# Optimization experiments

Hardware: AMD Instinct MI355X
Metric: run time of the kernel (lower is better)

The kernel has to match this reference:

```python
import jax, jax.numpy as jnp
import numpy as np

P1 = np.array([[1000.0, 0.0, 128.0, 64000.0],
               [0.0, 1000.0, 128.0, 64000.0],
               [0.0, 0.0, 1.0, 500.0]])
P2 = np.array([[-128.0, 0.0, 1000.0, 64000.0],
               [-128.0, 1000.0, 0.0, 64000.0],
               [-1.0, 0.0, 0.0, 500.0]])


def calculate_fundamental_matrix(P_src, P_dst):
    # l2 = F21 @ x1 : maps a point in P_src onto a line in P_dst
    C1 = -np.linalg.inv(P_src[:3, :3]) @ P_src[:3, 3]
    e = P_dst @ np.append(C1, 1.0)          # epipole of src camera center in dst view
    return np.cross(e, np.eye(3) * -1) @ P_dst @ np.linalg.pinv(P_src)


def setup_inputs() -> dict:
    key = jax.random.key(0)
    view1 = jax.random.normal(key, (8, 4, 256, 256), dtype=jnp.float32)
    F21 = calculate_fundamental_matrix(P1, P2).astype(np.float32)
    return {"view1": view1, "F": jnp.asarray(F21)}


def reference(view1, F):
    """Epipolar image translation: out(x2) = line integral of view1 along the
    epipolar line l1 = F^T @ x2 (bilinear sampling in v, unit steps in u,
    zero outside the image). Matches fume_torch_lib.translate semantics."""
    B, C, H, W = view1.shape
    dt = view1.dtype
    F = F.astype(dt)
    ys = jnp.arange(H, dtype=dt)[:, None]   # (H,1)
    xs = jnp.arange(W, dtype=dt)[None, :]   # (1,W)
    # line coefficients l = F^T @ [x, y, 1], per output pixel -> (H,W)
    a = F[0, 0] * xs + F[1, 0] * ys + F[2, 0]
    b = F[0, 1] * xs + F[1, 1] * ys + F[2, 1]
    c = F[0, 2] * xs + F[1, 2] * ys + F[2, 2]
    n = jnp.sqrt(a * a + b * b) + jnp.asarray(1e-12, dt)
    a, b, c = a / n, b / n, c / n
    ok = (jnp.abs(b) > 1e-6).astype(dt)                 # drop near-vertical lines
    b_safe = jnp.where(jnp.abs(b) > 1e-6, b, jnp.asarray(1.0, dt))

    def step(acc, u):
        uf = u.astype(dt)
        v = -(a * uf + c) / b_safe                      # (H,W) source row per out pixel
        v0 = jnp.floor(v)
        f = v - v0
        i0 = v0.astype(jnp.int32)
        i1 = i0 + 1
        m0 = ((i0 >= 0) & (i0 < H)).astype(dt)
        m1 = ((i1 >= 0) & (i1 < H)).astype(dt)
        col = jax.lax.dynamic_index_in_dim(view1, u, axis=3, keepdims=False)  # (B,C,H)
        s0 = col[:, :, jnp.clip(i0, 0, H - 1)]          # (B,C,H,W)
        s1 = col[:, :, jnp.clip(i1, 0, H - 1)]
        val = (s0 * (1.0 - f) * m0 + s1 * f * m1) * ok
        return acc + val, None

    out, _ = jax.lax.scan(step, jnp.zeros_like(view1), jnp.arange(W))
    return out
```

## Files before the change

### kernel.cpp

```cpp
#include <hip/hip_runtime.h>
#include <cstdint>

constexpr int Hh = 256, Ww = 256, BCc = 32;

constexpr int RBLK = 35;
constexpr int USTRIDE = RBLK * BCc * 8 * 2;
constexpr int UPLANES = 264;

constexpr int DW2    = 140;
constexpr int UROW2  = DW2 * BCc * 4;
constexpr size_t PSIZE = (size_t)UPLANES * UROW2;
constexpr size_t T5_BYTES = 2 * PSIZE;

typedef _Float16 half2v   __attribute__((ext_vector_type(2)));
typedef _Float16 half8v   __attribute__((ext_vector_type(8)));
typedef __fp16   fp16x2   __attribute__((ext_vector_type(2)));
typedef float    float16v __attribute__((ext_vector_type(16)));
typedef float    float4v  __attribute__((ext_vector_type(4)));
typedef uint32_t uint4v   __attribute__((ext_vector_type(4)));

static __device__ inline half2v pack2(float a, float b) {
    fp16x2 r = __builtin_amdgcn_cvt_pkrtz(a, b);
    return __builtin_bit_cast(half2v, r);
}

__global__ __launch_bounds__(256) void fume_pack2(const float* __restrict__ in,
                                                  char* __restrict__ P) {
    const int t   = threadIdx.x;
    const int bid = blockIdx.x;
    const int rt  = bid % 18;
    const int ut  = bid / 18;
    const int R0  = rt * 16;
    const int u0  = ut * 16;
    __shared__ float lds[32][17][17];

    for (int idx = t; idx < 32 * 17 * 4; idx += 256) {
        int q   = idx & 3;
        int rem = idx >> 2;
        int rl  = rem % 17;
        int ch  = rem / 17;
        int r   = R0 + rl - 8;
        int uq  = u0 + q * 4;
        float4v v = {0.f, 0.f, 0.f, 0.f};
        if ((unsigned)r < 256u && uq < 256)
            v = *(const float4v*)&in[ch * (Hh * Ww) + r * Ww + uq];
        lds[ch][rl][q * 4 + 0] = v[0];
        lds[ch][rl][q * 4 + 1] = v[1];
        lds[ch][rl][q * 4 + 2] = v[2];
        lds[ch][rl][q * 4 + 3] = v[3];
    }
    __syncthreads();

    for (int w = t; w < 8192; w += 256) {
        int ch    = w & 31;
        int rest  = w >> 5;
        int uu    = rest & 15;
        int rest2 = rest >> 4;
        int dd    = rest2 & 7;
        int p     = rest2 >> 3;
        int d     = (R0 >> 1) + dd;
        int u     = u0 + uu;
        if (d >= DW2 || u >= UPLANES) continue;
        int rl = 2 * dd + p;
        half2v pr = pack2(lds[ch][rl][uu], lds[ch][rl + 1][uu]);
        uint32_t wv;
        __builtin_memcpy(&wv, &pr, 4);
        *(uint32_t*)(P + (size_t)p * PSIZE + (size_t)u * UROW2
                     + d * 128 + ch * 4) = wv;
    }
}

__global__ __launch_bounds__(256, 8) void fume_mfma3(const char* __restrict__ P,
                                                     const float* __restrict__ Fm,
                                                     float* __restrict__ out) {
    __shared__ float red[4][32][33];
    const int t    = threadIdx.x;
    const int lane = t & 63;
    const int wq   = t >> 6;
    const int px   = lane & 31;
    const int h    = lane >> 5;
    const int bid  = (int)blockIdx.x;
    const int idx8 = bid >> 3;
    const int y    = ((bid & 7) << 5) + (idx8 >> 3);
    const int x0   = (idx8 & 7) * 32;
    const int x    = x0 + px;

    float xf = (float)x, yf = (float)y;
    float a = Fm[0] * xf + Fm[3] * yf + Fm[6];
    float b = Fm[1] * xf + Fm[4] * yf + Fm[7];
    float c = Fm[2] * xf + Fm[5] * yf + Fm[8];
    float n = sqrtf(a * a + b * b) + 1e-12f;
    a /= n; b /= n; c /= n;

    float alpha, beta_i;
    int u_lo, u_hi;
    if (fabsf(b) > 1e-6f) {
        alpha  = -a / b;
        beta_i = -c / b + 8.f;
        u_lo = 0; u_hi = Ww - 1;
        if (fabsf(alpha) > 1e-12f) {
            float inv = 1.f / alpha;
            float t0 = (7.f - beta_i) * inv;
            float t1 = (264.f - beta_i) * inv;
            int lo = (int)floorf(fminf(t0, t1));
            int hi = (int)ceilf (fmaxf(t0, t1));
            u_lo = lo > 0 ? lo : 0;
            u_hi = hi < (Ww - 1) ? hi : (Ww - 1);
        } else if (beta_i <= 7.f || beta_i >= 264.f) {
            u_lo = 1 << 20; u_hi = -(1 << 20);
        }
    } else {
        alpha = 0.f; beta_i = 3.0e4f;
        u_lo = 1 << 20; u_hi = -(1 << 20);
    }

    float xA = (float)x0, xB = (float)(x0 + 31);
    float aA = Fm[0] * xA + Fm[3] * yf + Fm[6];
    float bA = Fm[1] * xA + Fm[4] * yf + Fm[7];
    float cA = Fm[2] * xA + Fm[5] * yf + Fm[8];
    float aB = Fm[0] * xB + Fm[3] * yf + Fm[6];
    float bB = Fm[1] * xB + Fm[4] * yf + Fm[7];
    float cB = Fm[2] * xB + Fm[5] * yf + Fm[8];
    float alA = -aA / bA, beA = -cA / bA + 8.f;
    float alB = -aB / bB, beB = -cB / bB + 8.f;

    int lo = u_lo, hi = u_hi;
#pragma unroll
    for (int off = 1; off < 64; off <<= 1) {
        int l2 = __shfl_xor(lo, off, 64);
        int h2 = __shfl_xor(hi, off, 64);
        lo = lo < l2 ? lo : l2;
        hi = hi > h2 ? hi : h2;
    }
    lo = __builtin_amdgcn_readfirstlane(lo);
    hi = __builtin_amdgcn_readfirstlane(hi);

    float16v acc = {0.f, 0.f, 0.f, 0.f, 0.f, 0.f, 0.f, 0.f,
                    0.f, 0.f, 0.f, 0.f, 0.f, 0.f, 0.f, 0.f};

    if (lo <= hi) {
        int len = hi - lo + 1;
        int C   = (len + 3) >> 2;
        int cq  = (C + 3) >> 2;
        int nit = C - wq * cq;
        nit = nit < 0 ? 0 : (nit > cq ? cq : nit);
        int us  = lo + wq * cq * 4;

        int   u_l = us + lane;
        float uf  = (float)u_l;
        float vAl = fmaf(alA, uf, beA);
        float vBl = fmaf(alB, uf, beB);
        float mnu = fminf(vAl, vBl);
        float Mff = floorf(mnu - 0.01f);
        Mff = fmaxf(0.f, fminf(Mff, 272.f));
        int   Mi   = (int)Mff;
        int   pb   = Mi & 1;
        int   vOff = (pb ? (int)PSIZE : 0) + u_l * UROW2 + (Mi >> 1) * 128;
        int   vMfB = __builtin_bit_cast(int, Mff);

        float alpha2 = alpha + alpha;
        float vhh = fmaf(alpha, (float)(us + h), beta_i);
        const int chb = px << 2;

        uint32_t bA8[8], bB8[8], bC8[8];

#define FUME_ISS3(BUF, CH)                                                    \
    do {                                                                      \
        _Pragma("unroll")                                                     \
        for (int pr_ = 0; pr_ < 2; ++pr_) {                                   \
            int li_  = (CH) * 4 + 2 * pr_;                                    \
            int oe_  = __builtin_amdgcn_readlane(vOff, li_);                  \
            int oo_  = __builtin_amdgcn_readlane(vOff, li_ + 1);              \
            int sel_ = h ? oo_ : oe_;                                         \
            const char* q_ = P + (unsigned)(sel_ + chb);                      \
            _Pragma("unroll")                                                 \
            for (int k_ = 0; k_ < 4; ++k_)                                    \
                (BUF)[4 * pr_ + k_] = *(const uint32_t*)(q_ + 128 * k_);      \
        }                                                                     \
    } while (0)

#define FUME_COMP3(BUF, CH)                                                   \
    do {                                                                      \
        _Pragma("unroll")                                                     \
        for (int pr_ = 0; pr_ < 2; ++pr_) {                                   \
            int li_ = (CH) * 4 + 2 * pr_;                                     \
            int me_ = __builtin_amdgcn_readlane(vMfB, li_);                   \
            int mo_ = __builtin_amdgcn_readlane(vMfB, li_ + 1);               \
            float mf_ = __builtin_bit_cast(float, h ? mo_ : me_);             \
            float vbl_ = vhh - mf_;                                           \
            uint32_t aw_[4];                                                  \
            _Pragma("unroll")                                                 \
            for (int j_ = 0; j_ < 4; ++j_) {                                  \
                float d0_ = vbl_ - (float)(2 * j_);                           \
                float d1_ = vbl_ - (float)(2 * j_ + 1);                       \
                float t0_ = fmaxf(0.f, 1.f - fabsf(d0_));                     \
                float t1_ = fmaxf(0.f, 1.f - fabsf(d1_));                     \
                half2v tj_ = pack2(t0_, t1_);                                 \
                __builtin_memcpy(&aw_[j_], &tj_, 4);                          \
            }                                                                 \
            half8v A_;                                                        \
            __builtin_memcpy(&A_, aw_, 16);                                   \
            uint4v bw_ = {(BUF)[4 * pr_ + 0], (BUF)[4 * pr_ + 1],             \
                          (BUF)[4 * pr_ + 2], (BUF)[4 * pr_ + 3]};            \
            half8v B_ = __builtin_bit_cast(half8v, bw_);                      \
            acc = __builtin_amdgcn_mfma_f32_32x32x16_f16(A_, B_, acc, 0, 0, 0);\
            vhh += alpha2;                                                    \
        }                                                                     \
    } while (0)

        if (nit > 0) {
            FUME_ISS3(bA8, 0);
            if (nit > 1) FUME_ISS3(bB8, 1);
            int cc = 0;
            while (cc + 3 <= nit) {
                FUME_ISS3(bC8, cc + 2);
                FUME_COMP3(bA8, cc);
                int pf1 = (cc + 3 < nit) ? cc + 3 : nit - 1;
                FUME_ISS3(bA8, pf1);
                FUME_COMP3(bB8, cc + 1);
                int pf2 = (cc + 4 < nit) ? cc + 4 : nit - 1;
                FUME_ISS3(bB8, pf2);
                FUME_COMP3(bC8, cc + 2);
                cc += 3;
            }
            if (cc < nit) FUME_COMP3(bA8, cc);
            if (cc + 1 < nit) FUME_COMP3(bB8, cc + 1);
        }
#undef FUME_ISS3
#undef FUME_COMP3
    }

#pragma unroll
    for (int r = 0; r < 16; ++r) {
        int m = (r & 3) + 8 * (r >> 2) + 4 * h;
        red[wq][m][px] = acc[r];
    }
    __syncthreads();
    {
        int pxs = t & 31, cg = t >> 5;
#pragma unroll
        for (int jj = 0; jj < 4; ++jj) {
            int ch = cg + 8 * jj;
            float val = red[0][pxs][ch] + red[1][pxs][ch]
                      + red[2][pxs][ch] + red[3][pxs][ch];
            out[(size_t)ch * (Hh * Ww) + y * Ww + x0 + pxs] = val;
        }
    }
}

__global__ __launch_bounds__(256) void fume_pack(const float* __restrict__ in,
                                                 char* __restrict__ T4) {
    const int t   = threadIdx.x;
    const int bid = blockIdx.x;
    if (bid >= 512) {
        constexpr int NA = UPLANES * 3 * 32;
        constexpr int NB = 8 * 32 * 32;
        for (int id = (bid - 512) * 256 + t; id < NA + NB; id += 8 * 256) {
            int u, blk, ch;
            if (id < NA) {
                u = id / 96;
                int rem = id - u * 96;
                int bsel = rem >> 5;
                blk = (bsel == 0) ? 0 : (bsel == 1 ? 33 : 34);
                ch = rem & 31;
            } else {
                int id2 = id - NA;
                u = 256 + (id2 >> 10);
                int rem = id2 & 1023;
                blk = 1 + (rem >> 5);
                ch = rem & 31;
            }
            uint4v z = {0, 0, 0, 0};
            *(uint4v*)(T4 + (size_t)u * USTRIDE + blk * 512 + ch * 16) = z;
        }
        return;
    }
    __shared__ float lds[8][8][65];
    const int chg = bid & 3;
    const int r0  = ((bid >> 2) & 31) * 8;
    const int u0  = (bid >> 7) * 64;
    const int blk = (r0 >> 3) + 1;

#pragma unroll
    for (int it = 0; it < 16; ++it) {
        int idx = it * 256 + t;
        int ch = idx >> 9, rr = (idx >> 6) & 7, uu = idx & 63;
        lds[ch][rr][uu] =
            in[(chg * 8 + ch) * (Hh * Ww) + (r0 + rr) * Ww + u0 + uu];
    }
    __syncthreads();
    const int chl = t & 7;
#pragma unroll
    for (int p = 0; p < 2; ++p) {
        int u_l = (t >> 3) + p * 32;
        uint32_t w[4];
#pragma unroll
        for (int j = 0; j < 4; ++j) {
            half2v pr = pack2(lds[chl][2 * j][u_l], lds[chl][2 * j + 1][u_l]);
            __builtin_memcpy(&w[j], &pr, 4);
        }
        uint4v val = {w[0], w[1], w[2], w[3]};
        *(uint4v*)(T4 + (size_t)(u0 + u_l) * USTRIDE + blk * 512
                   + (chg * 8 + chl) * 16) = val;
    }
}

__global__ __launch_bounds__(256, 4) void fume_mfma(const char* __restrict__ T4,
                                                    const float* __restrict__ Fm,
                                                    float* __restrict__ out) {
    __shared__ float red[4][32][33];
    const int t    = threadIdx.x;
    const int lane = t & 63;
    const int wq   = t >> 6;
    const int px   = lane & 31;
    const int h    = lane >> 5;
    const int bid  = (int)blockIdx.x;
    const int idx8 = bid >> 3;
    const int y    = ((bid & 7) << 5) + (idx8 >> 3);
    const int x0   = (idx8 & 7) * 32;
    const int x    = x0 + px;

    float xf = (float)x, yf = (float)y;
    float a = Fm[0] * xf + Fm[3] * yf + Fm[6];
    float b = Fm[1] * xf + Fm[4] * yf + Fm[7];
    float c = Fm[2] * xf + Fm[5] * yf + Fm[8];
    float n = sqrtf(a * a + b * b) + 1e-12f;
    a /= n; b /= n; c /= n;

    float alpha, beta_i;
    int u_lo, u_hi;
    if (fabsf(b) > 1e-6f) {
        alpha  = -a / b;
        beta_i = -c / b + 8.f;
        u_lo = 0; u_hi = Ww - 1;
        if (fabsf(alpha) > 1e-12f) {
            float inv = 1.f / alpha;
            float t0 = (7.f - beta_i) * inv;
            float t1 = (264.f - beta_i) * inv;
            int lo = (int)floorf(fminf(t0, t1));
            int hi = (int)ceilf (fmaxf(t0, t1));
            u_lo = lo > 0 ? lo : 0;
            u_hi = hi < (Ww - 1) ? hi : (Ww - 1);
        } else if (beta_i <= 7.f || beta_i >= 264.f) {
            u_lo = 1 << 20; u_hi = -(1 << 20);
        }
    } else {
        alpha = 0.f; beta_i = 3.0e4f;
        u_lo = 1 << 20; u_hi = -(1 << 20);
    }

    float xA = (float)x0, xB = (float)(x0 + 31);
    float aA = Fm[0] * xA + Fm[3] * yf + Fm[6];
    float bA = Fm[1] * xA + Fm[4] * yf + Fm[7];
    float cA = Fm[2] * xA + Fm[5] * yf + Fm[8];
    float aB = Fm[0] * xB + Fm[3] * yf + Fm[6];
    float bB = Fm[1] * xB + Fm[4] * yf + Fm[7];
    float cB = Fm[2] * xB + Fm[5] * yf + Fm[8];
    float alA = -aA / bA, beA = -cA / bA + 8.f;
    float alB = -aB / bB, beB = -cB / bB + 8.f;

    int lo = u_lo, hi = u_hi;
#pragma unroll
    for (int off = 1; off < 64; off <<= 1) {
        int l2 = __shfl_xor(lo, off, 64);
        int h2 = __shfl_xor(hi, off, 64);
        lo = lo < l2 ? lo : l2;
        hi = hi > h2 ? hi : h2;
    }
    lo = __builtin_amdgcn_readfirstlane(lo);
    hi = __builtin_amdgcn_readfirstlane(hi);

    float16v acc = {0.f, 0.f, 0.f, 0.f, 0.f, 0.f, 0.f, 0.f,
                    0.f, 0.f, 0.f, 0.f, 0.f, 0.f, 0.f, 0.f};

    if (lo <= hi) {
        int len = hi - lo + 1;
        int C   = (len + 3) >> 2;
        int cq  = (C + 3) >> 2;
        int nit = C - wq * cq;
        nit = nit < 0 ? 0 : (nit > cq ? cq : nit);
        int n4  = nit << 2;
        int us  = lo + wq * cq * 4;

        float uf  = (float)(us + lane);
        float vAl = fmaf(alA, uf, beA);
        float vBl = fmaf(alB, uf, beB);
        float mnu = fminf(vAl, vBl);
        float Mf  = floorf(fmaf(mnu, 0.125f, -0.125f));
        Mf = fmaxf(0.f, fminf(Mf, 33.f));
        int   vMo  = (int)Mf << 9;
        float vB8f = Mf * 8.f;
        int   vB8i = __builtin_bit_cast(int, vB8f);

        float l8h = (float)(8 * h);
        float vh  = fmaf(alpha, (float)us, beta_i) - l8h;
        const char* pbq = T4 + (size_t)us * USTRIDE;
        const int voff  = (h << 9) + (px << 4);

        const half2v one2 = {(_Float16)1.f, (_Float16)1.f};

        for (int it2 = 0; it2 < n4; it2 += 4) {
#pragma unroll
            for (int i = 0; i < 4; ++i) {
                const int idx = it2 + i;
                int   Mo = __builtin_amdgcn_readlane(vMo, idx);
                float b8 = __builtin_bit_cast(
                    float, __builtin_amdgcn_readlane(vB8i, idx));
                uint4v bw = *(const uint4v*)(pbq + (size_t)idx * USTRIDE
                                             + (size_t)Mo + voff);
                float vbl = vh - b8;
                half2v vb2 = pack2(vbl, vbl);
                uint32_t aw[4];
#pragma unroll
                for (int j = 0; j < 4; ++j) {
                    half2v cj = {(_Float16)(float)(2 * j),
                                 (_Float16)(float)(2 * j + 1)};
                    half2v d  = vb2 - cj;
                    uint32_t du;
                    __builtin_memcpy(&du, &d, 4);
                    du &= 0x7fff7fffu;
                    half2v ad;
                    __builtin_memcpy(&ad, &du, 4);
                    half2v tj;
                    asm("v_pk_add_f16 %0, %1, %2 neg_lo:[0,1] neg_hi:[0,1] clamp"
                        : "=v"(tj)
                        : "v"(one2), "v"(ad));
                    __builtin_memcpy(&aw[j], &tj, 4);
                }
                half8v A;
                __builtin_memcpy(&A, aw, 16);
                half8v B = __builtin_bit_cast(half8v, bw);
                acc = __builtin_amdgcn_mfma_f32_32x32x16_f16(A, B, acc, 0, 0, 0);
                vh += alpha;
            }
        }
    }

#pragma unroll
    for (int r = 0; r < 16; ++r) {
        int m = (r & 3) + 8 * (r >> 2) + 4 * h;
        red[wq][m][px] = acc[r];
    }
    __syncthreads();
    {
        int pxs = t & 31, cg = t >> 5;
#pragma unroll
        for (int jj = 0; jj < 4; ++jj) {
            int ch = cg + 8 * jj;
            float val = red[0][pxs][ch] + red[1][pxs][ch]
                      + red[2][pxs][ch] + red[3][pxs][ch];
            out[(size_t)ch * (Hh * Ww) + y * Ww + x0 + pxs] = val;
        }
    }
}

__global__ __launch_bounds__(256) void fume_fallback(const float* __restrict__ src,
                                                     const float* __restrict__ Fm,
                                                     float* __restrict__ out) {
    int g = blockIdx.x * 256 + threadIdx.x;
    int part = g & 3;
    int pix  = g >> 2;
    int x = pix & (Ww - 1);
    int y = pix >> 8;
    int ch0 = part * 8;
    float xf = (float)x, yf = (float)y;
    float a = Fm[0] * xf + Fm[3] * yf + Fm[6];
    float b = Fm[1] * xf + Fm[4] * yf + Fm[7];
    float c = Fm[2] * xf + Fm[5] * yf + Fm[8];
    float n = sqrtf(a * a + b * b) + 1e-12f;
    a /= n; b /= n; c /= n;
    float acc[8];
#pragma unroll
    for (int k = 0; k < 8; ++k) acc[k] = 0.f;
    if (fabsf(b) > 1e-6f) {
        float alpha = -a / b, beta = -c / b;
        for (int u = 0; u < Ww; ++u) {
            float v  = fmaf(alpha, (float)u, beta);
            float rf = floorf(v);
            float f  = v - rf;
            int   ri = (int)rf;
            float w0 = ((unsigned)ri       < (unsigned)Hh) ? (1.f - f) : 0.f;
            float w1 = ((unsigned)(ri + 1) < (unsigned)Hh) ? f         : 0.f;
            int r0 = ri < 0 ? 0 : (ri > Hh - 1 ? Hh - 1 : ri);
            int r1 = ri + 1 < 0 ? 0 : (ri + 1 > Hh - 1 ? Hh - 1 : ri + 1);
#pragma unroll
            for (int k = 0; k < 8; ++k) {
                float s0 = src[(size_t)(ch0 + k) * (Hh * Ww) + r0 * Ww + u];
                float s1 = src[(size_t)(ch0 + k) * (Hh * Ww) + r1 * Ww + u];
                acc[k] = fmaf(w0, s0, fmaf(w1, s1, acc[k]));
            }
        }
    }
#pragma unroll
    for (int k = 0; k < 8; ++k)
        out[(size_t)(ch0 + k) * (Hh * Ww) + pix] = acc[k];
}

extern "C" void kernel_launch(void* const* d_in, const int* in_sizes, int n_in,
                              void* d_out, int out_size, void* d_ws, size_t ws_size,
                              hipStream_t stream) {
    const float* view1 = (const float*)d_in[0];
    const float* Fm    = (const float*)d_in[1];
    float* out = (float*)d_out;

    constexpr size_t t4_bytes = (size_t)UPLANES * USTRIDE;
    if (ws_size >= T5_BYTES) {
        char* P = (char*)d_ws;
        fume_pack2<<<306, 256, 0, stream>>>(view1, P);
        fume_mfma3<<<2048, 256, 0, stream>>>(P, Fm, out);
    } else if (ws_size >= t4_bytes) {
        char* T4 = (char*)d_ws;
        fume_pack<<<520, 256, 0, stream>>>(view1, T4);
        fume_mfma<<<2048, 256, 0, stream>>>(T4, Fm, out);
    } else {
        fume_fallback<<<(Hh * Ww * 4) / 256, 256, 0, stream>>>(view1, Fm, out);
    }
}
```

Before: 94.64 us.

## Replace triple-buffered load pipeline with simple loop and packed fp16 weight math

Removes the manual three-buffer software prefetch of B operands and iterates one MFMA pair per loop iteration with unrolling disabled, relying on hardware/compiler latency hiding and occupancy. The tent weights are now computed in packed fp16 (subtract, abs via mask, v_pk_add with clamp) instead of per-element fp32 ops followed by packing. This lowers VALU work and register pressure but exposes global/L2 load latency directly before each MFMA and computes the interpolation offsets in fp16, which loses precision for larger vbl values.

```diff
diff --git a/kernel.cpp b/kernel.cpp
--- a/kernel.cpp
+++ b/kernel.cpp
@@ -144,6 +144,7 @@
         int cq  = (C + 3) >> 2;
         int nit = C - wq * cq;
         nit = nit < 0 ? 0 : (nit > cq ? cq : nit);
+        int npair = nit << 1;
         int us  = lo + wq * cq * 4;
 
         int   u_l = us + lane;
@@ -162,72 +163,50 @@
         float vhh = fmaf(alpha, (float)(us + h), beta_i);
         const int chb = px << 2;
 
-        uint32_t bA8[8], bB8[8], bC8[8];
-
-#define FUME_ISS3(BUF, CH)                                                    \
-    do {                                                                      \
-        _Pragma("unroll")                                                     \
-        for (int pr_ = 0; pr_ < 2; ++pr_) {                                   \
-            int li_  = (CH) * 4 + 2 * pr_;                                    \
-            int oe_  = __builtin_amdgcn_readlane(vOff, li_);                  \
-            int oo_  = __builtin_amdgcn_readlane(vOff, li_ + 1);              \
-            int sel_ = h ? oo_ : oe_;                                         \
-            const char* q_ = P + (unsigned)(sel_ + chb);                      \
-            _Pragma("unroll")                                                 \
-            for (int k_ = 0; k_ < 4; ++k_)                                    \
-                (BUF)[4 * pr_ + k_] = *(const uint32_t*)(q_ + 128 * k_);      \
-        }                                                                     \
-    } while (0)
-
-#define FUME_COMP3(BUF, CH)                                                   \
-    do {                                                                      \
-        _Pragma("unroll")                                                     \
-        for (int pr_ = 0; pr_ < 2; ++pr_) {                                   \
-            int li_ = (CH) * 4 + 2 * pr_;                                     \
-            int me_ = __builtin_amdgcn_readlane(vMfB, li_);                   \
-            int mo_ = __builtin_amdgcn_readlane(vMfB, li_ + 1);               \
-            float mf_ = __builtin_bit_cast(float, h ? mo_ : me_);             \
-            float vbl_ = vhh - mf_;                                           \
-            uint32_t aw_[4];                                                  \
-            _Pragma("unroll")                                                 \
-            for (int j_ = 0; j_ < 4; ++j_) {                                  \
-                float d0_ = vbl_ - (float)(2 * j_);                           \
-                float d1_ = vbl_ - (float)(2 * j_ + 1);                       \
-                float t0_ = fmaxf(0.f, 1.f - fabsf(d0_));                     \
-                float t1_ = fmaxf(0.f, 1.f - fabsf(d1_));                     \
-                half2v tj_ = pack2(t0_, t1_);                                 \
-                __builtin_memcpy(&aw_[j_], &tj_, 4);                          \
-            }                                                                 \
-            half8v A_;                                                        \
-            __builtin_memcpy(&A_, aw_, 16);                                   \
-            uint4v bw_ = {(BUF)[4 * pr_ + 0], (BUF)[4 * pr_ + 1],             \
-                          (BUF)[4 * pr_ + 2], (BUF)[4 * pr_ + 3]};            \
-            half8v B_ = __builtin_bit_cast(half8v, bw_);                      \
-            acc = __builtin_amdgcn_mfma_f32_32x32x16_f16(A_, B_, acc, 0, 0, 0);\
-            vhh += alpha2;                                                    \
-        }                                                                     \
-    } while (0)
-
-        if (nit > 0) {
-            FUME_ISS3(bA8, 0);
-            if (nit > 1) FUME_ISS3(bB8, 1);
-            int cc = 0;
-            while (cc + 3 <= nit) {
-                FUME_ISS3(bC8, cc + 2);
-                FUME_COMP3(bA8, cc);
-                int pf1 = (cc + 3 < nit) ? cc + 3 : nit - 1;
-                FUME_ISS3(bA8, pf1);
-                FUME_COMP3(bB8, cc + 1);
-                int pf2 = (cc + 4 < nit) ? cc + 4 : nit - 1;
-                FUME_ISS3(bB8, pf2);
-                FUME_COMP3(bC8, cc + 2);
-                cc += 3;
+        const half2v one2 = {(_Float16)1.f, (_Float16)1.f};
+
+#pragma clang loop unroll(disable)
+        for (int pp = 0; pp < npair; ++pp) {
+            int oe  = __builtin_amdgcn_readlane(vOff, 2 * pp);
+            int oo  = __builtin_amdgcn_readlane(vOff, 2 * pp + 1);
+            int sel = h ? oo : oe;
+            const char* q = P + (unsigned)(sel + chb);
+            uint32_t b0 = *(const uint32_t*)(q);
+            uint32_t b1 = *(const uint32_t*)(q + 128);
+            uint32_t b2 = *(const uint32_t*)(q + 256);
+            uint32_t b3 = *(const uint32_t*)(q + 384);
+
+            int me = __builtin_amdgcn_readlane(vMfB, 2 * pp);
+            int mo = __builtin_amdgcn_readlane(vMfB, 2 * pp + 1);
+            float mf = __builtin_bit_cast(float, h ? mo : me);
+
+            float vbl = vhh - mf;
+            half2v vb2 = pack2(vbl, vbl);
+            uint32_t aw[4];
+#pragma unroll
+            for (int j = 0; j < 4; ++j) {
+                half2v cj = {(_Float16)(float)(2 * j),
+                             (_Float16)(float)(2 * j + 1)};
+                half2v d  = vb2 - cj;
+                uint32_t du;
+                __builtin_memcpy(&du, &d, 4);
+                du &= 0x7fff7fffu;
+                half2v ad;
+                __builtin_memcpy(&ad, &du, 4);
+                half2v tj;
+                asm("v_pk_add_f16 %0, %1, %2 neg_lo:[0,1] neg_hi:[0,1] clamp"
+                    : "=v"(tj)
+                    : "v"(one2), "v"(ad));
+                __builtin_memcpy(&aw[j], &tj, 4);
             }
-            if (cc < nit) FUME_COMP3(bA8, cc);
-            if (cc + 1 < nit) FUME_COMP3(bB8, cc + 1);
-        }
-#undef FUME_ISS3
-#undef FUME_COMP3
+            half8v A;
+            __builtin_memcpy(&A, aw, 16);
+            uint4v bw = {b0, b1, b2, b3};
+            half8v B = __builtin_bit_cast(half8v, bw);
+            acc = __builtin_amdgcn_mfma_f32_32x32x16_f16(A, B, acc, 0, 0, 0);
+
+            vhh += alpha2;
+        }
     }
 
 #pragma unroll
```

Measured after the change: 94.96 us. Within noise of the previous version (+0.3%).
